# Optimization experiments

Measured on AMD Instinct MI355X. Metric: run time of the kernel, lower is better.

## Reference

```python
import jax, jax.numpy as jnp
import numpy as np

BLOCK_K = 128  # per_1x128 block quantization: block_n=1 (per row), block_k=128


def _dequant(wq, scale):
    # wq: [E, N, K] quantized codes; scale: [E, N, ceil(K/BLOCK_K)]
    K = wq.shape[-1]
    s_full = jnp.repeat(scale, BLOCK_K, axis=-1)[..., :K]
    return wq * s_full


def setup_inputs() -> dict:
    key = jax.random.key(0)
    ks = jax.random.split(key, 6)
    T, E, H, I = 1024, 8, 1024, 768
    x = jax.random.normal(ks[0], (T, H), dtype=jnp.float32)
    router_logits = jax.random.normal(ks[1], (T, E), dtype=jnp.float32)
    # fp8 codes simulated as float values; block scales positive (scale_inv)
    w13_weight = jax.random.normal(ks[2], (E, 2 * I, H), dtype=jnp.float32) * 0.05
    w13_weight_scale_inv = jax.random.uniform(ks[3], (E, 2 * I, H // BLOCK_K), dtype=jnp.float32, minval=0.5, maxval=1.5)
    w2_weight = jax.random.normal(ks[4], (E, H, I), dtype=jnp.float32) * 0.05
    w2_weight_scale_inv = jax.random.uniform(ks[5], (E, H, I // BLOCK_K), dtype=jnp.float32, minval=0.5, maxval=1.5)
    return {
        "x": x,
        "router_logits": router_logits,
        "w13_weight": w13_weight,
        "w13_weight_scale_inv": w13_weight_scale_inv,
        "w2_weight": w2_weight,
        "w2_weight_scale_inv": w2_weight_scale_inv,
        "top_k": 2,
    }


def reference(x, router_logits, w13_weight, w13_weight_scale_inv, w2_weight, w2_weight_scale_inv, top_k):
    T, H = x.shape
    E = router_logits.shape[-1]
    I = w2_weight.shape[-1]

    # ---- dequantize block-scaled weights (inline dequant of fp8 grouped GEMM) ----
    w13 = _dequant(w13_weight, w13_weight_scale_inv)   # [E, 2I, H]
    w2 = _dequant(w2_weight, w2_weight_scale_inv)      # [E, H, I]

    # ---- routing: softmax scoring, top_k, renormalize ----
    probs = jax.nn.softmax(router_logits, axis=-1)     # [T, E]
    topk_w, topk_idx = jax.lax.top_k(probs, top_k)     # [T, K]
    topk_w = topk_w / jnp.sum(topk_w, axis=-1, keepdims=True)  # renormalize=True
    # dense combine weights [T, E] (scatter of top_k routing weights)
    combine = jnp.zeros((T, E), x.dtype).at[jnp.arange(T)[:, None], topk_idx].add(topk_w)

    # ---- grouped expert FFN (dense-over-experts reference) ----
    gate_up = jnp.einsum('th,enh->ten', x, w13)        # [T, E, 2I]
    gate, up = gate_up[..., :I], gate_up[..., I:]
    act = jax.nn.silu(gate) * up                       # silu activation ('silu')
    out_e = jnp.einsum('tei,ehi->teh', act, w2)        # [T, E, H]

    # ---- combine ----
    return jnp.einsum('teh,te->th', out_e, combine)    # [T, H]
```

## Files before the change

### kernel.cpp

```cpp
#include <hip/hip_runtime.h>

#define T_TOK 1024
#define H_DIM 1024
#define I_DIM 768
#define E_NUM 8

#define G13 1572864
#define G2   786432
#define GX   131072

typedef __bf16 bf16x8 __attribute__((ext_vector_type(8)));
typedef float  f32x4  __attribute__((ext_vector_type(4)));

__device__ inline bf16x8 cvt8(float4 a, float4 b, float s) {
    bf16x8 o;
    o[0] = (__bf16)(a.x * s); o[1] = (__bf16)(a.y * s);
    o[2] = (__bf16)(a.z * s); o[3] = (__bf16)(a.w * s);
    o[4] = (__bf16)(b.x * s); o[5] = (__bf16)(b.y * s);
    o[6] = (__bf16)(b.z * s); o[7] = (__bf16)(b.w * s);
    return o;
}

__global__ __launch_bounds__(256) void prep_kernel(
    const float* __restrict__ w13, const float* __restrict__ w13s,
    const float* __restrict__ w2,  const float* __restrict__ w2s,
    const float* __restrict__ x,   float4* __restrict__ out4,
    __bf16* __restrict__ w13d, __bf16* __restrict__ w2d, __bf16* __restrict__ xbf)
{
    int g = blockIdx.x * 256 + threadIdx.x;
    if (g < G13) {
        int k8 = g & 127;
        int row = g >> 7;
        float s = w13s[(row << 3) | (k8 >> 4)];
        const float4* src = (const float4*)w13 + (size_t)g * 2;
        *(bf16x8*)(w13d + (size_t)g * 8) = cvt8(src[0], src[1], s);
    } else if (g < G13 + G2) {
        int g2 = g - G13;
        unsigned row = (unsigned)g2 / 96u;
        int k8 = g2 - row * 96;
        float s = w2s[row * 6 + (k8 >> 4)];
        const float4* src = (const float4*)w2 + (size_t)g2 * 2;
        *(bf16x8*)(w2d + (size_t)g2 * 8) = cvt8(src[0], src[1], s);
    } else if (g < G13 + G2 + GX) {
        int gx = g - (G13 + G2);
        const float4* src = (const float4*)x + (size_t)gx * 2;
        *(bf16x8*)(xbf + (size_t)gx * 8) = cvt8(src[0], src[1], 1.0f);
    } else {
        int go = g - (G13 + G2 + GX);
        float4 z = make_float4(0.f, 0.f, 0.f, 0.f);
        out4[2 * go] = z; out4[2 * go + 1] = z;
    }
}

__global__ __launch_bounds__(1024) void router_kernel(
    const float* __restrict__ logits,
    int* __restrict__ counts, int* __restrict__ base,
    int* __restrict__ tok_list, float* __restrict__ wt_list)
{
    __shared__ int cnt[E_NUM];
    const int t = threadIdx.x;
    if (t < E_NUM) cnt[t] = 0;
    __syncthreads();
    float l[E_NUM];
#pragma unroll
    for (int e = 0; e < E_NUM; e++) l[e] = logits[t * E_NUM + e];
    int e0 = 0; float m0 = l[0];
#pragma unroll
    for (int e = 1; e < E_NUM; e++) if (l[e] > m0) { m0 = l[e]; e0 = e; }
    int e1 = -1; float m1 = -3e38f;
#pragma unroll
    for (int e = 0; e < E_NUM; e++) if (e != e0 && l[e] > m1) { m1 = l[e]; e1 = e; }
    float w0 = 1.0f / (1.0f + expf(m1 - m0));
    float w1 = 1.0f - w0;
    int p0 = atomicAdd(&cnt[e0], 1);
    tok_list[e0 * T_TOK + p0] = t;
    wt_list[e0 * T_TOK + p0] = w0;
    int p1 = atomicAdd(&cnt[e1], 1);
    tok_list[e1 * T_TOK + p1] = t;
    wt_list[e1 * T_TOK + p1] = w1;
    __syncthreads();
    if (t == 0) {
        int s = 0;
        for (int e = 0; e < E_NUM; e++) { base[e] = s; counts[e] = cnt[e]; s += cnt[e]; }
    }
}

#define MFMA(A, B, C) __builtin_amdgcn_mfma_f32_16x16x32_bf16(A, B, C, 0, 0, 0)

struct Stage { uint4 a, b0, b1, b2, b3; };

__device__ inline Stage ld_stage(const __bf16* pA, const __bf16* pB, int k) {
    Stage s;
    s.a  = *(const uint4*)(pA + k);
    s.b0 = *(const uint4*)(pB + k);
    s.b1 = *(const uint4*)(pB + k + 8);
    s.b2 = *(const uint4*)(pB + k + 16);
    s.b3 = *(const uint4*)(pB + k + 24);
    return s;
}

__device__ inline void st_stage(char* As, char* Bs, int awo,
                                int bw0, int bw1, int bw2, int bw3,
                                const Stage& s) {
    *(uint4*)(As + awo) = s.a;
    *(uint4*)(Bs + bw0) = s.b0;
    *(uint4*)(Bs + bw1) = s.b1;
    *(uint4*)(Bs + bw2) = s.b2;
    *(uint4*)(Bs + bw3) = s.b3;
}

__global__ __launch_bounds__(256, 4) void gemm1_kernel(
    const __bf16* __restrict__ xbf,
    const __bf16* __restrict__ w13d,
    const int* __restrict__ counts,
    const int* __restrict__ base,
    const int* __restrict__ tok_list,
    __bf16* __restrict__ act)
{
    const int e = blockIdx.z;
    const int count = counts[e];
    const int m0 = blockIdx.y * 32;
    if (m0 >= count) return;
    const int n0 = blockIdx.x * 64;
    const int abase = base[e];

    __shared__ union {
        struct { __bf16 Bs[2][128 * 64]; __bf16 As[2][32 * 64]; } s;
        float gu[32 * 132];
        int tok[32];
    } u;

    const int tid = threadIdx.x;
    if (tid < 32) {
        int r = m0 + tid;
        u.tok[tid] = (r < count) ? tok_list[e * T_TOK + r] : tok_list[e * T_TOK];
    }
    __syncthreads();
    const int arow = tid >> 3, ag = tid & 7;
    const int tok_a = u.tok[arow];
    __syncthreads();

    const __bf16* pA = xbf + (size_t)tok_a * H_DIM + ag * 8;
    const int awo = arow * 128 + ((ag ^ (arow & 7)) << 4);
    const int brow = tid >> 1, bg0 = (tid & 1) * 4;
    const int nB = (brow < 64) ? (n0 + brow) : (I_DIM + n0 + brow - 64);
    const __bf16* pB = w13d + ((size_t)e * 2 * I_DIM + nB) * H_DIM + bg0 * 8;
    const int bw0 = brow * 128 + (((bg0 + 0) ^ (brow & 7)) << 4);
    const int bw1 = brow * 128 + (((bg0 + 1) ^ (brow & 7)) << 4);
    const int bw2 = brow * 128 + (((bg0 + 2) ^ (brow & 7)) << 4);
    const int bw3 = brow * 128 + (((bg0 + 3) ^ (brow & 7)) << 4);

    const int wid = tid >> 6, lane = tid & 63, lrow = lane & 15, quad = lane >> 4;
    int aoff[2][2], boff[2][2];
#pragma unroll
    for (int kk = 0; kk < 2; kk++) {
        int gph = ((kk * 4 + quad) ^ (lrow & 7)) << 4;
#pragma unroll
        for (int i = 0; i < 2; i++) {
            aoff[kk][i] = (i * 16 + lrow) * 128 + gph;
            boff[kk][i] = (wid * 32 + i * 16 + lrow) * 128 + gph;
        }
    }

    f32x4 acc[2][2];
#pragma unroll
    for (int i = 0; i < 2; i++)
#pragma unroll
        for (int j = 0; j < 2; j++) { f32x4 z = {0.f, 0.f, 0.f, 0.f}; acc[i][j] = z; }

    char* A0 = (char*)u.s.As[0]; char* A1 = (char*)u.s.As[1];
    char* B0 = (char*)u.s.Bs[0]; char* B1 = (char*)u.s.Bs[1];

    auto compute = [&](const char* Ab, const char* Bb) {
#pragma unroll
        for (int kk = 0; kk < 2; kk++) {
            bf16x8 a0 = *(const bf16x8*)(Ab + aoff[kk][0]);
            bf16x8 a1 = *(const bf16x8*)(Ab + aoff[kk][1]);
            bf16x8 b0 = *(const bf16x8*)(Bb + boff[kk][0]);
            bf16x8 b1 = *(const bf16x8*)(Bb + boff[kk][1]);
            acc[0][0] = MFMA(a0, b0, acc[0][0]);
            acc[1][0] = MFMA(a1, b0, acc[1][0]);
            acc[0][1] = MFMA(a0, b1, acc[0][1]);
            acc[1][1] = MFMA(a1, b1, acc[1][1]);
        }
    };

    Stage X = ld_stage(pA, pB, 0);
    Stage Y = ld_stage(pA, pB, 64);
    st_stage(A0, B0, awo, bw0, bw1, bw2, bw3, X);
    X = ld_stage(pA, pB, 2 * 64);
    __syncthreads();

#pragma unroll
    for (int uu = 0; uu < 8; ++uu) {
        st_stage(A1, B1, awo, bw0, bw1, bw2, bw3, Y);
        if (2 * uu + 3 < 16) Y = ld_stage(pA, pB, (2 * uu + 3) * 64);
        compute(A0, B0);
        __syncthreads();
        if (uu < 7) st_stage(A0, B0, awo, bw0, bw1, bw2, bw3, X);
        if (2 * uu + 4 < 16) X = ld_stage(pA, pB, (2 * uu + 4) * 64);
        compute(A1, B1);
        __syncthreads();
    }

#pragma unroll
    for (int i = 0; i < 2; i++)
#pragma unroll
        for (int j = 0; j < 2; j++)
#pragma unroll
            for (int r = 0; r < 4; r++) {
                int m = i * 16 + quad * 4 + r;
                int c = wid * 32 + j * 16 + lrow;
                u.gu[m * 132 + c] = acc[i][j][r];
            }
    __syncthreads();

#pragma unroll
    for (int ii = 0; ii < 8; ii++) {
        int o = ii * 256 + tid;
        int m = o >> 6, c = o & 63;
        if (m0 + m < count) {
            float g  = u.gu[m * 132 + c];
            float up = u.gu[m * 132 + 64 + c];
            float a  = g / (1.0f + expf(-g)) * up;
            act[(size_t)(abase + m0 + m) * I_DIM + n0 + c] = (__bf16)a;
        }
    }
}

__global__ __launch_bounds__(256, 4) void gemm2_kernel(
    const __bf16* __restrict__ act,
    const __bf16* __restrict__ w2d,
    const int* __restrict__ counts,
    const int* __restrict__ base,
    const int* __restrict__ tok_list,
    const float* __restrict__ wt_list,
    float* __restrict__ out)
{
    const int e = blockIdx.z;
    const int count = counts[e];
    const int m0 = blockIdx.y * 32;
    if (m0 >= count) return;
    const int n0 = blockIdx.x * 128;
    const int abase = base[e];

    __shared__ struct { __bf16 Bs[2][128 * 64]; __bf16 As[2][32 * 64]; } s;

    const int tid = threadIdx.x;
    const int arow = tid >> 3, ag = tid & 7;
    int gr = abase + m0 + arow;
    if (gr > 2 * T_TOK - 1) gr = 2 * T_TOK - 1;
    const __bf16* pA = act + (size_t)gr * I_DIM + ag * 8;
    const int awo = arow * 128 + ((ag ^ (arow & 7)) << 4);

    const int brow = tid >> 1, bg0 = (tid & 1) * 4;
    const __bf16* pB = w2d + ((size_t)e * H_DIM + n0 + brow) * I_DIM + bg0 * 8;
    const int bw0 = brow * 128 + (((bg0 + 0) ^ (brow & 7)) << 4);
    const int bw1 = brow * 128 + (((bg0 + 1) ^ (brow & 7)) << 4);
    const int bw2 = brow * 128 + (((bg0 + 2) ^ (brow & 7)) << 4);
    const int bw3 = brow * 128 + (((bg0 + 3) ^ (brow & 7)) << 4);

    const int wid = tid >> 6, lane = tid & 63, lrow = lane & 15, quad = lane >> 4;
    int aoff[2][2], boff[2][2];
#pragma unroll
    for (int kk = 0; kk < 2; kk++) {
        int gph = ((kk * 4 + quad) ^ (lrow & 7)) << 4;
#pragma unroll
        for (int i = 0; i < 2; i++) {
            aoff[kk][i] = (i * 16 + lrow) * 128 + gph;
            boff[kk][i] = (wid * 32 + i * 16 + lrow) * 128 + gph;
        }
    }

    f32x4 acc[2][2];
#pragma unroll
    for (int i = 0; i < 2; i++)
#pragma unroll
        for (int j = 0; j < 2; j++) { f32x4 z = {0.f, 0.f, 0.f, 0.f}; acc[i][j] = z; }

    char* A0 = (char*)s.As[0]; char* A1 = (char*)s.As[1];
    char* B0 = (char*)s.Bs[0]; char* B1 = (char*)s.Bs[1];

    auto compute = [&](const char* Ab, const char* Bb) {
#pragma unroll
        for (int kk = 0; kk < 2; kk++) {
            bf16x8 a0 = *(const bf16x8*)(Ab + aoff[kk][0]);
            bf16x8 a1 = *(const bf16x8*)(Ab + aoff[kk][1]);
            bf16x8 b0 = *(const bf16x8*)(Bb + boff[kk][0]);
            bf16x8 b1 = *(const bf16x8*)(Bb + boff[kk][1]);
            acc[0][0] = MFMA(a0, b0, acc[0][0]);
            acc[1][0] = MFMA(a1, b0, acc[1][0]);
            acc[0][1] = MFMA(a0, b1, acc[0][1]);
            acc[1][1] = MFMA(a1, b1, acc[1][1]);
        }
    };

    Stage X = ld_stage(pA, pB, 0);
    Stage Y = ld_stage(pA, pB, 64);
    st_stage(A0, B0, awo, bw0, bw1, bw2, bw3, X);
    X = ld_stage(pA, pB, 2 * 64);
    __syncthreads();

#pragma unroll
    for (int uu = 0; uu < 6; ++uu) {
        st_stage(A1, B1, awo, bw0, bw1, bw2, bw3, Y);
        if (2 * uu + 3 < 12) Y = ld_stage(pA, pB, (2 * uu + 3) * 64);
        compute(A0, B0);
        __syncthreads();
        if (uu < 5) st_stage(A0, B0, awo, bw0, bw1, bw2, bw3, X);
        if (2 * uu + 4 < 12) X = ld_stage(pA, pB, (2 * uu + 4) * 64);
        compute(A1, B1);
        __syncthreads();
    }

#pragma unroll
    for (int i = 0; i < 2; i++)
#pragma unroll
        for (int r = 0; r < 4; r++) {
            int m = i * 16 + quad * 4 + r;
            if (m0 + m < count) {
                int   t = tok_list[e * T_TOK + m0 + m];
                float w = wt_list[e * T_TOK + m0 + m];
#pragma unroll
                for (int j = 0; j < 2; j++) {
                    int h = n0 + wid * 32 + j * 16 + lrow;
                    atomicAdd(&out[(size_t)t * H_DIM + h], w * acc[i][j][r]);
                }
            }
        }
}

extern "C" void kernel_launch(void* const* d_in, const int* in_sizes, int n_in,
                              void* d_out, int out_size, void* d_ws, size_t ws_size,
                              hipStream_t stream) {
    (void)in_sizes; (void)n_in; (void)out_size; (void)ws_size;
    const float* x      = (const float*)d_in[0];
    const float* logits = (const float*)d_in[1];
    const float* w13    = (const float*)d_in[2];
    const float* w13s   = (const float*)d_in[3];
    const float* w2     = (const float*)d_in[4];
    const float* w2s    = (const float*)d_in[5];
    float* out = (float*)d_out;

    char* ws = (char*)d_ws;
    int*    counts   = (int*)ws;
    int*    base     = (int*)(ws + 128);
    int*    tok_list = (int*)(ws + 256);
    float*  wt_list  = (float*)(ws + 256 + 32768);
    __bf16* act      = (__bf16*)(ws + 65792);
    __bf16* xbf      = (__bf16*)(ws + 65792 + 3145728);
    __bf16* w13d     = (__bf16*)(ws + 65792 + 3145728 + 2097152);
    __bf16* w2d      = (__bf16*)(ws + 65792 + 3145728 + 2097152 + 25165824);

    prep_kernel<<<dim3(10240), 256, 0, stream>>>(w13, w13s, w2, w2s, x,
                                                 (float4*)out, w13d, w2d, xbf);
    router_kernel<<<dim3(1), 1024, 0, stream>>>(logits, counts, base, tok_list, wt_list);
    gemm1_kernel<<<dim3(I_DIM / 64, T_TOK / 32, E_NUM), 256, 0, stream>>>(
        xbf, w13d, counts, base, tok_list, act);
    gemm2_kernel<<<dim3(H_DIM / 128, T_TOK / 32, E_NUM), 256, 0, stream>>>(
        act, w2d, counts, base, tok_list, wt_list, out);
}
```

Baseline: 166.1 us.

## Double M tile to 64 rows and remap blocks for XCD-local weight reuse

Both grouped GEMMs now compute 64 token rows per block instead of 32, so each weight tile loaded from global memory is reused across twice as many rows and fewer blocks re-read the weights. The 3D grid is flattened to 1D with a remap that places blocks of the same expert and N-tile on the same XCD, aiming for better L2 locality. The cost is twice the accumulator registers and more LDS per block, so launch bounds drop to 3 waves per SIMD. More rows are also wasted on experts whose token count is not a multiple of 64.

```diff
diff --git a/kernel.cpp b/kernel.cpp
--- a/kernel.cpp
+++ b/kernel.cpp
@@ -87,11 +87,13 @@
 
 #define MFMA(A, B, C) __builtin_amdgcn_mfma_f32_16x16x32_bf16(A, B, C, 0, 0, 0)
 
-struct Stage { uint4 a, b0, b1, b2, b3; };
-
-__device__ inline Stage ld_stage(const __bf16* pA, const __bf16* pB, int k) {
+struct Stage { uint4 a0, a1, b0, b1, b2, b3; };
+
+__device__ inline Stage ld_stage(const __bf16* pA0, const __bf16* pA1,
+                                 const __bf16* pB, int k) {
     Stage s;
-    s.a  = *(const uint4*)(pA + k);
+    s.a0 = *(const uint4*)(pA0 + k);
+    s.a1 = *(const uint4*)(pA1 + k);
     s.b0 = *(const uint4*)(pB + k);
     s.b1 = *(const uint4*)(pB + k + 8);
     s.b2 = *(const uint4*)(pB + k + 16);
@@ -99,17 +101,18 @@
     return s;
 }
 
-__device__ inline void st_stage(char* As, char* Bs, int awo,
+__device__ inline void st_stage(char* As, char* Bs, int aw0, int aw1,
                                 int bw0, int bw1, int bw2, int bw3,
                                 const Stage& s) {
-    *(uint4*)(As + awo) = s.a;
+    *(uint4*)(As + aw0) = s.a0;
+    *(uint4*)(As + aw1) = s.a1;
     *(uint4*)(Bs + bw0) = s.b0;
     *(uint4*)(Bs + bw1) = s.b1;
     *(uint4*)(Bs + bw2) = s.b2;
     *(uint4*)(Bs + bw3) = s.b3;
 }
 
-__global__ __launch_bounds__(256, 4) void gemm1_kernel(
+__global__ __launch_bounds__(256, 3) void gemm1_kernel(
     const __bf16* __restrict__ xbf,
     const __bf16* __restrict__ w13d,
     const int* __restrict__ counts,
@@ -117,31 +120,35 @@
     const int* __restrict__ tok_list,
     __bf16* __restrict__ act)
 {
-    const int e = blockIdx.z;
+    const int bx = blockIdx.x;
+    const int xcd = bx & 7, t = bx >> 3;
+    const int p = t % 12, m = t / 12;
+    const int P = xcd + 8 * p;
+    const int nb = P % 12, e = P / 12;
     const int count = counts[e];
-    const int m0 = blockIdx.y * 32;
+    const int m0 = m * 64;
     if (m0 >= count) return;
-    const int n0 = blockIdx.x * 64;
+    const int n0 = nb * 64;
     const int abase = base[e];
 
     __shared__ union {
-        struct { __bf16 Bs[2][128 * 64]; __bf16 As[2][32 * 64]; } s;
-        float gu[32 * 132];
-        int tok[32];
+        struct { __bf16 Bs[2][128 * 64]; __bf16 As[2][64 * 64]; } s;
+        float gu[64 * 132];
     } u;
+    __shared__ int tokS[64];
 
     const int tid = threadIdx.x;
-    if (tid < 32) {
+    if (tid < 64) {
         int r = m0 + tid;
-        u.tok[tid] = (r < count) ? tok_list[e * T_TOK + r] : tok_list[e * T_TOK];
-    }
-    __syncthreads();
+        tokS[tid] = (r < count) ? tok_list[e * T_TOK + r] : tok_list[e * T_TOK];
+    }
+    __syncthreads();
+
     const int arow = tid >> 3, ag = tid & 7;
-    const int tok_a = u.tok[arow];
-    __syncthreads();
-
-    const __bf16* pA = xbf + (size_t)tok_a * H_DIM + ag * 8;
-    const int awo = arow * 128 + ((ag ^ (arow & 7)) << 4);
+    const __bf16* pA0 = xbf + (size_t)tokS[arow] * H_DIM + ag * 8;
+    const __bf16* pA1 = xbf + (size_t)tokS[arow + 32] * H_DIM + ag * 8;
+    const int aw0 = arow * 128 + ((ag ^ (arow & 7)) << 4);
+    const int aw1 = aw0 + 32 * 128;
     const int brow = tid >> 1, bg0 = (tid & 1) * 4;
     const int nB = (brow < 64) ? (n0 + brow) : (I_DIM + n0 + brow - 64);
     const __bf16* pB = w13d + ((size_t)e * 2 * I_DIM + nB) * H_DIM + bg0 * 8;
@@ -151,20 +158,19 @@
     const int bw3 = brow * 128 + (((bg0 + 3) ^ (brow & 7)) << 4);
 
     const int wid = tid >> 6, lane = tid & 63, lrow = lane & 15, quad = lane >> 4;
-    int aoff[2][2], boff[2][2];
+    int aoff[2][4], boff[2][2];
 #pragma unroll
     for (int kk = 0; kk < 2; kk++) {
         int gph = ((kk * 4 + quad) ^ (lrow & 7)) << 4;
 #pragma unroll
-        for (int i = 0; i < 2; i++) {
-            aoff[kk][i] = (i * 16 + lrow) * 128 + gph;
-            boff[kk][i] = (wid * 32 + i * 16 + lrow) * 128 + gph;
-        }
-    }
-
-    f32x4 acc[2][2];
-#pragma unroll
-    for (int i = 0; i < 2; i++)
+        for (int i = 0; i < 4; i++) aoff[kk][i] = (i * 16 + lrow) * 128 + gph;
+#pragma unroll
+        for (int j = 0; j < 2; j++) boff[kk][j] = (wid * 32 + j * 16 + lrow) * 128 + gph;
+    }
+
+    f32x4 acc[4][2];
+#pragma unroll
+    for (int i = 0; i < 4; i++)
 #pragma unroll
         for (int j = 0; j < 2; j++) { f32x4 z = {0.f, 0.f, 0.f, 0.f}; acc[i][j] = z; }
 
@@ -174,61 +180,61 @@
     auto compute = [&](const char* Ab, const char* Bb) {
 #pragma unroll
         for (int kk = 0; kk < 2; kk++) {
-            bf16x8 a0 = *(const bf16x8*)(Ab + aoff[kk][0]);
-            bf16x8 a1 = *(const bf16x8*)(Ab + aoff[kk][1]);
             bf16x8 b0 = *(const bf16x8*)(Bb + boff[kk][0]);
             bf16x8 b1 = *(const bf16x8*)(Bb + boff[kk][1]);
-            acc[0][0] = MFMA(a0, b0, acc[0][0]);
-            acc[1][0] = MFMA(a1, b0, acc[1][0]);
-            acc[0][1] = MFMA(a0, b1, acc[0][1]);
-            acc[1][1] = MFMA(a1, b1, acc[1][1]);
+#pragma unroll
+            for (int i = 0; i < 4; i++) {
+                bf16x8 a = *(const bf16x8*)(Ab + aoff[kk][i]);
+                acc[i][0] = MFMA(a, b0, acc[i][0]);
+                acc[i][1] = MFMA(a, b1, acc[i][1]);
+            }
         }
     };
 
-    Stage X = ld_stage(pA, pB, 0);
-    Stage Y = ld_stage(pA, pB, 64);
-    st_stage(A0, B0, awo, bw0, bw1, bw2, bw3, X);
-    X = ld_stage(pA, pB, 2 * 64);
+    Stage X = ld_stage(pA0, pA1, pB, 0);
+    Stage Y = ld_stage(pA0, pA1, pB, 64);
+    st_stage(A0, B0, aw0, aw1, bw0, bw1, bw2, bw3, X);
+    X = ld_stage(pA0, pA1, pB, 2 * 64);
     __syncthreads();
 
 #pragma unroll
     for (int uu = 0; uu < 8; ++uu) {
-        st_stage(A1, B1, awo, bw0, bw1, bw2, bw3, Y);
-        if (2 * uu + 3 < 16) Y = ld_stage(pA, pB, (2 * uu + 3) * 64);
+        st_stage(A1, B1, aw0, aw1, bw0, bw1, bw2, bw3, Y);
+        if (2 * uu + 3 < 16) Y = ld_stage(pA0, pA1, pB, (2 * uu + 3) * 64);
         compute(A0, B0);
         __syncthreads();
-        if (uu < 7) st_stage(A0, B0, awo, bw0, bw1, bw2, bw3, X);
-        if (2 * uu + 4 < 16) X = ld_stage(pA, pB, (2 * uu + 4) * 64);
+        if (uu < 7) st_stage(A0, B0, aw0, aw1, bw0, bw1, bw2, bw3, X);
+        if (2 * uu + 4 < 16) X = ld_stage(pA0, pA1, pB, (2 * uu + 4) * 64);
         compute(A1, B1);
         __syncthreads();
     }
 
 #pragma unroll
-    for (int i = 0; i < 2; i++)
+    for (int i = 0; i < 4; i++)
 #pragma unroll
         for (int j = 0; j < 2; j++)
 #pragma unroll
             for (int r = 0; r < 4; r++) {
-                int m = i * 16 + quad * 4 + r;
+                int mr = i * 16 + quad * 4 + r;
                 int c = wid * 32 + j * 16 + lrow;
-                u.gu[m * 132 + c] = acc[i][j][r];
+                u.gu[mr * 132 + c] = acc[i][j][r];
             }
     __syncthreads();
 
 #pragma unroll
-    for (int ii = 0; ii < 8; ii++) {
+    for (int ii = 0; ii < 16; ii++) {
         int o = ii * 256 + tid;
-        int m = o >> 6, c = o & 63;
-        if (m0 + m < count) {
-            float g  = u.gu[m * 132 + c];
-            float up = u.gu[m * 132 + 64 + c];
+        int mr = o >> 6, c = o & 63;
+        if (m0 + mr < count) {
+            float g  = u.gu[mr * 132 + c];
+            float up = u.gu[mr * 132 + 64 + c];
             float a  = g / (1.0f + expf(-g)) * up;
-            act[(size_t)(abase + m0 + m) * I_DIM + n0 + c] = (__bf16)a;
+            act[(size_t)(abase + m0 + mr) * I_DIM + n0 + c] = (__bf16)a;
         }
     }
 }
 
-__global__ __launch_bounds__(256, 4) void gemm2_kernel(
+__global__ __launch_bounds__(256, 3) void gemm2_kernel(
     const __bf16* __restrict__ act,
     const __bf16* __restrict__ w2d,
     const int* __restrict__ counts,
@@ -237,21 +243,27 @@
     const float* __restrict__ wt_list,
     float* __restrict__ out)
 {
-    const int e = blockIdx.z;
+    const int bx = blockIdx.x;
+    const int xcd = bx & 7, t = bx >> 3;
+    const int p = t & 7, m = t >> 3;
+    const int P = xcd + 8 * p;
+    const int nb = P & 7, e = P >> 3;
     const int count = counts[e];
-    const int m0 = blockIdx.y * 32;
+    const int m0 = m * 64;
     if (m0 >= count) return;
-    const int n0 = blockIdx.x * 128;
+    const int n0 = nb * 128;
     const int abase = base[e];
 
-    __shared__ struct { __bf16 Bs[2][128 * 64]; __bf16 As[2][32 * 64]; } s;
+    __shared__ struct { __bf16 Bs[2][128 * 64]; __bf16 As[2][64 * 64]; } s;
 
     const int tid = threadIdx.x;
     const int arow = tid >> 3, ag = tid & 7;
-    int gr = abase + m0 + arow;
-    if (gr > 2 * T_TOK - 1) gr = 2 * T_TOK - 1;
-    const __bf16* pA = act + (size_t)gr * I_DIM + ag * 8;
-    const int awo = arow * 128 + ((ag ^ (arow & 7)) << 4);
+    int gr0 = abase + m0 + arow;      if (gr0 > 2 * T_TOK - 1) gr0 = 2 * T_TOK - 1;
+    int gr1 = abase + m0 + arow + 32; if (gr1 > 2 * T_TOK - 1) gr1 = 2 * T_TOK - 1;
+    const __bf16* pA0 = act + (size_t)gr0 * I_DIM + ag * 8;
+    const __bf16* pA1 = act + (size_t)gr1 * I_DIM + ag * 8;
+    const int aw0 = arow * 128 + ((ag ^ (arow & 7)) << 4);
+    const int aw1 = aw0 + 32 * 128;
 
     const int brow = tid >> 1, bg0 = (tid & 1) * 4;
     const __bf16* pB = w2d + ((size_t)e * H_DIM + n0 + brow) * I_DIM + bg0 * 8;
@@ -261,20 +273,19 @@
     const int bw3 = brow * 128 + (((bg0 + 3) ^ (brow & 7)) << 4);
 
     const int wid = tid >> 6, lane = tid & 63, lrow = lane & 15, quad = lane >> 4;
-    int aoff[2][2], boff[2][2];
+    int aoff[2][4], boff[2][2];
 #pragma unroll
     for (int kk = 0; kk < 2; kk++) {
         int gph = ((kk * 4 + quad) ^ (lrow & 7)) << 4;
 #pragma unroll
-        for (int i = 0; i < 2; i++) {
-            aoff[kk][i] = (i * 16 + lrow) * 128 + gph;
-            boff[kk][i] = (wid * 32 + i * 16 + lrow) * 128 + gph;
-        }
-    }
-
-    f32x4 acc[2][2];
-#pragma unroll
-    for (int i = 0; i < 2; i++)
+        for (int i = 0; i < 4; i++) aoff[kk][i] = (i * 16 + lrow) * 128 + gph;
+#pragma unroll
+        for (int j = 0; j < 2; j++) boff[kk][j] = (wid * 32 + j * 16 + lrow) * 128 + gph;
+    }
+
+    f32x4 acc[4][2];
+#pragma unroll
+    for (int i = 0; i < 4; i++)
 #pragma unroll
         for (int j = 0; j < 2; j++) { f32x4 z = {0.f, 0.f, 0.f, 0.f}; acc[i][j] = z; }
 
@@ -284,47 +295,47 @@
     auto compute = [&](const char* Ab, const char* Bb) {
 #pragma unroll
         for (int kk = 0; kk < 2; kk++) {
-            bf16x8 a0 = *(const bf16x8*)(Ab + aoff[kk][0]);
-            bf16x8 a1 = *(const bf16x8*)(Ab + aoff[kk][1]);
             bf16x8 b0 = *(const bf16x8*)(Bb + boff[kk][0]);
             bf16x8 b1 = *(const bf16x8*)(Bb + boff[kk][1]);
-            acc[0][0] = MFMA(a0, b0, acc[0][0]);
-            acc[1][0] = MFMA(a1, b0, acc[1][0]);
-            acc[0][1] = MFMA(a0, b1, acc[0][1]);
-            acc[1][1] = MFMA(a1, b1, acc[1][1]);
+#pragma unroll
+            for (int i = 0; i < 4; i++) {
+                bf16x8 a = *(const bf16x8*)(Ab + aoff[kk][i]);
+                acc[i][0] = MFMA(a, b0, acc[i][0]);
+                acc[i][1] = MFMA(a, b1, acc[i][1]);
+            }
         }
     };
 
-    Stage X = ld_stage(pA, pB, 0);
-    Stage Y = ld_stage(pA, pB, 64);
-    st_stage(A0, B0, awo, bw0, bw1, bw2, bw3, X);
-    X = ld_stage(pA, pB, 2 * 64);
+    Stage X = ld_stage(pA0, pA1, pB, 0);
+    Stage Y = ld_stage(pA0, pA1, pB, 64);
+    st_stage(A0, B0, aw0, aw1, bw0, bw1, bw2, bw3, X);
+    X = ld_stage(pA0, pA1, pB, 2 * 64);
     __syncthreads();
 
 #pragma unroll
     for (int uu = 0; uu < 6; ++uu) {
-        st_stage(A1, B1, awo, bw0, bw1, bw2, bw3, Y);
-        if (2 * uu + 3 < 12) Y = ld_stage(pA, pB, (2 * uu + 3) * 64);
+        st_stage(A1, B1, aw0, aw1, bw0, bw1, bw2, bw3, Y);
+        if (2 * uu + 3 < 12) Y = ld_stage(pA0, pA1, pB, (2 * uu + 3) * 64);
         compute(A0, B0);
         __syncthreads();
-        if (uu < 5) st_stage(A0, B0, awo, bw0, bw1, bw2, bw3, X);
-        if (2 * uu + 4 < 12) X = ld_stage(pA, pB, (2 * uu + 4) * 64);
+        if (uu < 5) st_stage(A0, B0, aw0, aw1, bw0, bw1, bw2, bw3, X);
+        if (2 * uu + 4 < 12) X = ld_stage(pA0, pA1, pB, (2 * uu + 4) * 64);
         compute(A1, B1);
         __syncthreads();
     }
 
 #pragma unroll
-    for (int i = 0; i < 2; i++)
+    for (int i = 0; i < 4; i++)
 #pragma unroll
         for (int r = 0; r < 4; r++) {
-            int m = i * 16 + quad * 4 + r;
-            if (m0 + m < count) {
-                int   t = tok_list[e * T_TOK + m0 + m];
-                float w = wt_list[e * T_TOK + m0 + m];
+            int mr = i * 16 + quad * 4 + r;
+            if (m0 + mr < count) {
+                int   tk = tok_list[e * T_TOK + m0 + mr];
+                float w  = wt_list[e * T_TOK + m0 + mr];
 #pragma unroll
                 for (int j = 0; j < 2; j++) {
                     int h = n0 + wid * 32 + j * 16 + lrow;
-                    atomicAdd(&out[(size_t)t * H_DIM + h], w * acc[i][j][r]);
+                    atomicAdd(&out[(size_t)tk * H_DIM + h], w * acc[i][j][r]);
                 }
             }
         }
@@ -355,8 +366,8 @@
     prep_kernel<<<dim3(10240), 256, 0, stream>>>(w13, w13s, w2, w2s, x,
                                                  (float4*)out, w13d, w2d, xbf);
     router_kernel<<<dim3(1), 1024, 0, stream>>>(logits, counts, base, tok_list, wt_list);
-    gemm1_kernel<<<dim3(I_DIM / 64, T_TOK / 32, E_NUM), 256, 0, stream>>>(
+    gemm1_kernel<<<dim3(1536), 256, 0, stream>>>(
         xbf, w13d, counts, base, tok_list, act);
-    gemm2_kernel<<<dim3(H_DIM / 128, T_TOK / 32, E_NUM), 256, 0, stream>>>(
+    gemm2_kernel<<<dim3(1024), 256, 0, stream>>>(
         act, w2d, counts, base, tok_list, wt_list, out);
 }
```

Measured after the change: 154.1 us. 1.08x faster.
